# Optimization experiments

Hardware: AMD Instinct MI355X
Metric: run time of the kernel (lower is better)

Reference implementation:

```python
import jax, jax.numpy as jnp
import numpy as np

N = 128        # n_neurons == neuron_dim (required by einsum 'bdn,ijn')
IN_FEAT = 4608  # grid_size**2 * embed_dim_doubled = 9 * 512
B = 32          # batch(4) * num_candidates(8)


def setup_inputs() -> dict:
    key = jax.random.key(0)
    ks = jax.random.split(key, 8)
    s_in = 1.0 / np.sqrt(IN_FEAT)
    s_d = 1.0 / np.sqrt(N)
    return {
        "x": jax.random.normal(ks[0], (B, IN_FEAT), jnp.float32),
        "input_proj_w": jax.random.uniform(ks[1], (N, IN_FEAT), jnp.float32, -s_in, s_in),
        "input_proj_b": jax.random.uniform(ks[2], (N,), jnp.float32, -s_in, s_in),
        "neuron_states": jax.random.normal(ks[3], (N, N), jnp.float32),
        "edge_vectors": jax.random.normal(ks[4], (N, N, N), jnp.float32),
        "recreate_w": jax.random.uniform(ks[5], (IN_FEAT, N), jnp.float32, -s_d, s_d),
        "recreate_b": jnp.zeros((IN_FEAT,), jnp.float32),
        "score_w": jax.random.uniform(ks[6], (1, N), jnp.float32, -s_d, s_d),
        "score_b": jnp.zeros((1,), jnp.float32),
        "grid_size": 3,
        "num_candidates": 8,
        "n_steps": 2,
    }


def reference(x, input_proj_w, input_proj_b, neuron_states, edge_vectors,
              recreate_w, recreate_b, score_w, score_b,
              grid_size, num_candidates, n_steps):
    bc = x.shape[0]                                   # batch * num_candidates
    embed_dim_doubled = x.shape[1] // (grid_size ** 2)
    n = neuron_states.shape[0]                        # == neuron_dim

    x_t = x @ input_proj_w.T + input_proj_b          # (B, d)
    # neuron_states: (n, d) -> states: (B, d, n), input added per feature channel
    states = neuron_states.T[None, :, :] + x_t[:, :, None]
    mask = 1.0 - jnp.eye(n, dtype=x.dtype)            # (n, n), no self term

    for _ in range(n_steps):
        # (B,d,n) x (n,n,n) -> (B,d,i,j): the O(B*d*n^2) intermediate
        T = jnp.einsum('bdn,ijn->bdij', states, edge_vectors)
        messages = jnp.einsum('bdij,bdn->bdi', T, states)  # (B, d, n)
        # literal broadcast of mask (1,n,n) against (B,d,n); valid since d==n
        messages = messages * mask[None, :, :]
        states = jax.nn.relu(messages)                     # (B, d, n)

    out = states[:, :, -1]                                 # (B, d)
    recreation = out @ recreate_w.T + recreate_b           # (B, IN_FEAT)
    scores = out @ score_w.T + score_b                     # (B, 1)

    bsz = bc // num_candidates
    recreation = recreation.reshape(bsz, num_candidates, grid_size ** 2, embed_dim_doubled)
    scores = scores.reshape(bsz, num_candidates)
    return recreation, scores
```

## Files before the change

### kernel.cpp

```cpp
#include <hip/hip_runtime.h>


#define KQ 1152

__device__ __forceinline__ float wave_reduce64(float v) {
#pragma unroll
  for (int m = 32; m >= 1; m >>= 1) v += __shfl_xor(v, m);
  return v;
}

#define WS_EJP 0
#define WS_XT 65536
#define WS_OBD 69632

__global__ __launch_bounds__(256) void k1_pre(const float* __restrict__ ev,
                                              const float* __restrict__ x,
                                              const float* __restrict__ ipw,
                                              const float* __restrict__ ipb,
                                              float* __restrict__ ws) {
  int tid = threadIdx.x, blk = blockIdx.x;
  if (blk < 512) {
    __shared__ __align__(16) float4 sarr[256];
    int i = blk >> 2, jc = blk & 3;
    int n4 = tid & 31, jg = tid >> 5;
    const float4* ev4 = (const float4*)ev;
    float4 acc = make_float4(0.f, 0.f, 0.f, 0.f);
#pragma unroll
    for (int jj = 0; jj < 4; ++jj) {
      int j = jc * 32 + jj * 8 + jg;
      float4 v = ev4[i * 4096 + j * 32 + n4];
      acc.x += v.x; acc.y += v.y; acc.z += v.z; acc.w += v.w;
    }
    sarr[tid] = acc;
    __syncthreads();
    if (tid < 32) {
      float4 s = sarr[tid];
#pragma unroll
      for (int k = 1; k < 8; ++k) {
        float4 v = sarr[tid + 32 * k];
        s.x += v.x; s.y += v.y; s.z += v.z; s.w += v.w;
      }
      ((float4*)(ws + WS_EJP))[(jc * 128 + i) * 32 + tid] = s;
    }
  } else {
    int gw = (blk - 512) * 4 + (tid >> 6);
    int lane = tid & 63;
    int b0 = (gw >> 6) << 1, d0 = (gw & 63) << 1;
    const float4* x4 = (const float4*)x;
    const float4* w4 = (const float4*)ipw;
    float a00 = 0.f, a01 = 0.f, a10 = 0.f, a11 = 0.f;
#pragma unroll 6
    for (int kq = lane; kq < KQ; kq += 64) {
      float4 xa = x4[b0 * KQ + kq];
      float4 xb = x4[(b0 + 1) * KQ + kq];
      float4 wa = w4[d0 * KQ + kq];
      float4 wb = w4[(d0 + 1) * KQ + kq];
      a00 += xa.x * wa.x + xa.y * wa.y + xa.z * wa.z + xa.w * wa.w;
      a01 += xa.x * wb.x + xa.y * wb.y + xa.z * wb.z + xa.w * wb.w;
      a10 += xb.x * wa.x + xb.y * wa.y + xb.z * wa.z + xb.w * wa.w;
      a11 += xb.x * wb.x + xb.y * wb.y + xb.z * wb.z + xb.w * wb.w;
    }
    a00 = wave_reduce64(a00);
    a01 = wave_reduce64(a01);
    a10 = wave_reduce64(a10);
    a11 = wave_reduce64(a11);
    if (lane == 0) {
      float* xt = ws + WS_XT;
      xt[b0 * 128 + d0] = a00 + ipb[d0];
      xt[b0 * 128 + d0 + 1] = a01 + ipb[d0 + 1];
      xt[(b0 + 1) * 128 + d0] = a10 + ipb[d0];
      xt[(b0 + 1) * 128 + d0 + 1] = a11 + ipb[d0 + 1];
    }
  }
}

#define EJS 129
__global__ __launch_bounds__(256) void k2_fused(const float* __restrict__ ns,
                                                float* __restrict__ ws) {
  __shared__ float ej[128 * EJS];
  __shared__ float nscol[128];
  __shared__ float at2[2][128], e2[2][128];
  __shared__ float At[128], Ev[128];
  __shared__ float xts[32];
  __shared__ float csum_s;
  int tid = threadIdx.x, d = blockIdx.x;
  if (tid < 128) nscol[tid] = ns[tid * 128 + d];
  else if (tid < 160) xts[tid - 128] = (ws + WS_XT)[(tid - 128) * 128 + d];
  {
    int i = tid >> 1, h = tid & 1;
    const float4* p0 = (const float4*)(ws + WS_EJP) + i * 32 + h * 16;
#pragma unroll
    for (int w = 0; w < 16; ++w) {
      float4 v0 = p0[w];
      float4 v1 = p0[4096 + w];
      float4 v2 = p0[8192 + w];
      float4 v3 = p0[12288 + w];
      float* dst = &ej[i * EJS + h * 64 + w * 4];
      dst[0] = v0.x + v1.x + v2.x + v3.x;
      dst[1] = v0.y + v1.y + v2.y + v3.y;
      dst[2] = v0.z + v1.z + v2.z + v3.z;
      dst[3] = v0.w + v1.w + v2.w + v3.w;
    }
  }
  __syncthreads();
  {
    int i = tid & 127, h = tid >> 7;
    float a = 0.f, es = 0.f;
    const float* ejr = &ej[i * EJS + h * 64];
    const float* nsr = &nscol[h * 64];
#pragma unroll 8
    for (int n = 0; n < 64; ++n) {
      float v = ejr[n];
      a += v * nsr[n];
      es += v;
    }
    at2[h][i] = a;
    e2[h][i] = es;
  }
  if (tid < 64) {
    float cl = nscol[tid] + nscol[tid + 64];
    cl = wave_reduce64(cl);
    if (tid == 0) csum_s = cl;
  }
  __syncthreads();
  if (tid < 128) {
    At[tid] = at2[0][tid] + at2[1][tid];
    Ev[tid] = e2[0][tid] + e2[1][tid];
  }
  __syncthreads();
  float csum = csum_s;
  int wv = tid >> 6, l = tid & 63;
  const float* ej127 = &ej[127 * EJS];
  float* obd = ws + WS_OBD;
#pragma unroll
  for (int bb = 0; bb < 8; ++bb) {
    int b = wv * 8 + bb;
    float t = xts[b];
    float s0s = csum + 128.f * t;
    float sig = 0.f, y = 0.f;
#pragma unroll
    for (int m = 0; m < 2; ++m) {
      int i = l + (m << 6);
      float v = s0s * (At[i] + t * Ev[i]);
      v = (i == d) ? 0.f : v;
      v = fmaxf(v, 0.f);
      sig += v;
      y += ej127[i] * v;
    }
    sig = wave_reduce64(sig);
    y = wave_reduce64(y);
    if (l == 0) {
      float m2 = sig * y;
      if (d == 127) m2 = 0.f;
      obd[b * 128 + d] = fmaxf(m2, 0.f);
    }
  }
}

__global__ __launch_bounds__(256) void k3_proj(const float* __restrict__ rw,
                                               const float* __restrict__ rb,
                                               const float* __restrict__ sw,
                                               const float* __restrict__ sb,
                                               const float* __restrict__ ws,
                                               float* __restrict__ out) {
  const float* obd = ws + WS_OBD;
  int tid = threadIdx.x;
  int blk = blockIdx.x;
  if (blk < 144) {
    __shared__ __align__(16) float rwlds[32 * 136];
    __shared__ float obdT[128 * 33];
    int f0 = blk * 32;
    const float4* rw4 = (const float4*)rw;
#pragma unroll
    for (int it = 0; it < 4; ++it) {
      int q = tid + 256 * it;
      int f = q >> 5, n4 = q & 31;
      *(float4*)&rwlds[f * 136 + n4 * 4] = rw4[f0 * 32 + q];
    }
#pragma unroll
    for (int it = 0; it < 16; ++it) {
      int q = tid + 256 * it;
      int b = q >> 7, d = q & 127;
      obdT[d * 33 + b] = obd[q];
    }
    __syncthreads();
    int f = tid >> 3, bg = tid & 7;
    float acc[4] = {0.f, 0.f, 0.f, 0.f};
#pragma unroll 4
    for (int d = 0; d < 128; ++d) {
      float w = rwlds[f * 136 + d];
#pragma unroll
      for (int k = 0; k < 4; ++k) acc[k] += w * obdT[d * 33 + bg * 4 + k];
    }
    float bias = rb[f0 + f];
#pragma unroll
    for (int k = 0; k < 4; ++k) out[(bg * 4 + k) * 4608 + f0 + f] = acc[k] + bias;
  } else {
    int b = tid >> 3, l8 = tid & 7;
    float acc = 0.f;
    for (int d = l8; d < 128; d += 8) acc += obd[b * 128 + d] * sw[d];
    acc += __shfl_xor(acc, 1);
    acc += __shfl_xor(acc, 2);
    acc += __shfl_xor(acc, 4);
    if (l8 == 0) out[147456 + b] = acc + sb[0];
  }
}

extern "C" void kernel_launch(void* const* d_in, const int* in_sizes, int n_in,
                              void* d_out, int out_size, void* d_ws, size_t ws_size,
                              hipStream_t stream) {
  const float* x   = (const float*)d_in[0];
  const float* ipw = (const float*)d_in[1];
  const float* ipb = (const float*)d_in[2];
  const float* ns  = (const float*)d_in[3];
  const float* ev  = (const float*)d_in[4];
  const float* rw  = (const float*)d_in[5];
  const float* rb  = (const float*)d_in[6];
  const float* sw  = (const float*)d_in[7];
  const float* sb  = (const float*)d_in[8];
  float* out = (float*)d_out;
  float* ws = (float*)d_ws;

  k1_pre<<<768, 256, 0, stream>>>(ev, x, ipw, ipb, ws);
  k2_fused<<<128, 256, 0, stream>>>(ns, ws);
  k3_proj<<<145, 256, 0, stream>>>(rw, rb, sw, sb, ws, out);
}
```

Measured before the change: 107.1 us.

## Finalize edge-vector j-reduction in pre-kernel and precompute transposed sums for brain kernel

The pre-kernel now reduces the full j axis of edge_vectors per i in one block instead of four partial blocks. It writes a transposed ej matrix, per-row sums and row 127 directly to workspace. The middle kernel drops its per-block reload and summation of four partial slabs into LDS. It reads the transposed matrix from global with coalesced columns and uses precomputed sums. This removes redundant per-d work but leaves fewer blocks streaming the large edge tensor, and the transposed stores are strided.

```diff
diff --git a/kernel.cpp b/kernel.cpp
--- a/kernel.cpp
+++ b/kernel.cpp
@@ -8,10 +8,17 @@
   for (int m = 32; m >= 1; m >>= 1) v += __shfl_xor(v, m);
   return v;
 }
-
-#define WS_EJP 0
-#define WS_XT 65536
-#define WS_OBD 69632
+__device__ __forceinline__ float wave_reduce32(float v) {
+#pragma unroll
+  for (int m = 16; m >= 1; m >>= 1) v += __shfl_xor(v, m);
+  return v;
+}
+
+#define WS_EJT 0
+#define WS_E 16384
+#define WS_EJ127 16512
+#define WS_XT 16640
+#define WS_OBD 20736
 
 __global__ __launch_bounds__(256) void k1_pre(const float* __restrict__ ev,
                                               const float* __restrict__ x,
@@ -19,15 +26,15 @@
                                               const float* __restrict__ ipb,
                                               float* __restrict__ ws) {
   int tid = threadIdx.x, blk = blockIdx.x;
-  if (blk < 512) {
+  if (blk < 128) {
     __shared__ __align__(16) float4 sarr[256];
-    int i = blk >> 2, jc = blk & 3;
+    int i = blk;
     int n4 = tid & 31, jg = tid >> 5;
     const float4* ev4 = (const float4*)ev;
     float4 acc = make_float4(0.f, 0.f, 0.f, 0.f);
 #pragma unroll
-    for (int jj = 0; jj < 4; ++jj) {
-      int j = jc * 32 + jj * 8 + jg;
+    for (int jj = 0; jj < 16; ++jj) {
+      int j = jg * 16 + jj;
       float4 v = ev4[i * 4096 + j * 32 + n4];
       acc.x += v.x; acc.y += v.y; acc.z += v.z; acc.w += v.w;
     }
@@ -40,10 +47,19 @@
         float4 v = sarr[tid + 32 * k];
         s.x += v.x; s.y += v.y; s.z += v.z; s.w += v.w;
       }
-      ((float4*)(ws + WS_EJP))[(jc * 128 + i) * 32 + tid] = s;
+      float* EJT = ws + WS_EJT;
+      int n0 = tid * 4;
+      EJT[(n0 + 0) * 128 + i] = s.x;
+      EJT[(n0 + 1) * 128 + i] = s.y;
+      EJT[(n0 + 2) * 128 + i] = s.z;
+      EJT[(n0 + 3) * 128 + i] = s.w;
+      if (i == 127) *(float4*)(ws + WS_EJ127 + n0) = s;
+      float p = s.x + s.y + s.z + s.w;
+      p = wave_reduce32(p);
+      if (tid == 0) (ws + WS_E)[i] = p;
     }
   } else {
-    int gw = (blk - 512) * 4 + (tid >> 6);
+    int gw = (blk - 128) * 4 + (tid >> 6);
     int lane = tid & 63;
     int b0 = (gw >> 6) << 1, d0 = (gw & 63) << 1;
     const float4* x4 = (const float4*)x;
@@ -74,48 +90,22 @@
   }
 }
 
-#define EJS 129
-__global__ __launch_bounds__(256) void k2_fused(const float* __restrict__ ns,
+__global__ __launch_bounds__(256) void k2_brain(const float* __restrict__ ns,
                                                 float* __restrict__ ws) {
-  __shared__ float ej[128 * EJS];
-  __shared__ float nscol[128];
-  __shared__ float at2[2][128], e2[2][128];
-  __shared__ float At[128], Ev[128];
-  __shared__ float xts[32];
+  __shared__ float nscol[128], xts[32], at2[2][128], Atf[128];
   __shared__ float csum_s;
   int tid = threadIdx.x, d = blockIdx.x;
   if (tid < 128) nscol[tid] = ns[tid * 128 + d];
   else if (tid < 160) xts[tid - 128] = (ws + WS_XT)[(tid - 128) * 128 + d];
-  {
-    int i = tid >> 1, h = tid & 1;
-    const float4* p0 = (const float4*)(ws + WS_EJP) + i * 32 + h * 16;
-#pragma unroll
-    for (int w = 0; w < 16; ++w) {
-      float4 v0 = p0[w];
-      float4 v1 = p0[4096 + w];
-      float4 v2 = p0[8192 + w];
-      float4 v3 = p0[12288 + w];
-      float* dst = &ej[i * EJS + h * 64 + w * 4];
-      dst[0] = v0.x + v1.x + v2.x + v3.x;
-      dst[1] = v0.y + v1.y + v2.y + v3.y;
-      dst[2] = v0.z + v1.z + v2.z + v3.z;
-      dst[3] = v0.w + v1.w + v2.w + v3.w;
-    }
-  }
   __syncthreads();
   {
     int i = tid & 127, h = tid >> 7;
-    float a = 0.f, es = 0.f;
-    const float* ejr = &ej[i * EJS + h * 64];
+    const float* EJTp = ws + WS_EJT + h * 64 * 128 + i;
     const float* nsr = &nscol[h * 64];
+    float a = 0.f;
 #pragma unroll 8
-    for (int n = 0; n < 64; ++n) {
-      float v = ejr[n];
-      a += v * nsr[n];
-      es += v;
-    }
+    for (int n = 0; n < 64; ++n) a += EJTp[n * 128] * nsr[n];
     at2[h][i] = a;
-    e2[h][i] = es;
   }
   if (tid < 64) {
     float cl = nscol[tid] + nscol[tid + 64];
@@ -123,32 +113,26 @@
     if (tid == 0) csum_s = cl;
   }
   __syncthreads();
-  if (tid < 128) {
-    At[tid] = at2[0][tid] + at2[1][tid];
-    Ev[tid] = e2[0][tid] + e2[1][tid];
-  }
+  if (tid < 128) Atf[tid] = at2[0][tid] + at2[1][tid];
   __syncthreads();
+  int wv = tid >> 6, l = tid & 63;
+  float a0 = Atf[l], a1 = Atf[l + 64];
+  float e0 = (ws + WS_E)[l], e1 = (ws + WS_E)[l + 64];
+  float q0 = (ws + WS_EJ127)[l], q1 = (ws + WS_EJ127)[l + 64];
   float csum = csum_s;
-  int wv = tid >> 6, l = tid & 63;
-  const float* ej127 = &ej[127 * EJS];
+  bool z0 = (l == d), z1 = (l + 64 == d);
   float* obd = ws + WS_OBD;
 #pragma unroll
   for (int bb = 0; bb < 8; ++bb) {
     int b = wv * 8 + bb;
     float t = xts[b];
     float s0s = csum + 128.f * t;
-    float sig = 0.f, y = 0.f;
-#pragma unroll
-    for (int m = 0; m < 2; ++m) {
-      int i = l + (m << 6);
-      float v = s0s * (At[i] + t * Ev[i]);
-      v = (i == d) ? 0.f : v;
-      v = fmaxf(v, 0.f);
-      sig += v;
-      y += ej127[i] * v;
-    }
-    sig = wave_reduce64(sig);
-    y = wave_reduce64(y);
+    float v0 = s0s * (a0 + t * e0);
+    float v1 = s0s * (a1 + t * e1);
+    v0 = z0 ? 0.f : fmaxf(v0, 0.f);
+    v1 = z1 ? 0.f : fmaxf(v1, 0.f);
+    float sig = wave_reduce64(v0 + v1);
+    float y = wave_reduce64(q0 * v0 + q1 * v1);
     if (l == 0) {
       float m2 = sig * y;
       if (d == 127) m2 = 0.f;
@@ -180,8 +164,8 @@
 #pragma unroll
     for (int it = 0; it < 16; ++it) {
       int q = tid + 256 * it;
-      int b = q >> 7, d = q & 127;
-      obdT[d * 33 + b] = obd[q];
+      int b = q >> 7, dd = q & 127;
+      obdT[dd * 33 + b] = obd[q];
     }
     __syncthreads();
     int f = tid >> 3, bg = tid & 7;
@@ -221,7 +205,7 @@
   float* out = (float*)d_out;
   float* ws = (float*)d_ws;
 
-  k1_pre<<<768, 256, 0, stream>>>(ev, x, ipw, ipb, ws);
-  k2_fused<<<128, 256, 0, stream>>>(ns, ws);
+  k1_pre<<<384, 256, 0, stream>>>(ev, x, ipw, ipb, ws);
+  k2_brain<<<128, 256, 0, stream>>>(ns, ws);
   k3_proj<<<145, 256, 0, stream>>>(rw, rb, sw, sb, ws, out);
 }
```

Measured after the change: 99.23 us. 7.3% less time.
